# Kernel tuning notes

Measured on AMD Instinct MI355X. Metric: run time of the kernel, lower is better.

## Reference

```python
import jax, jax.numpy as jnp
import numpy as np


def setup_inputs() -> dict:
    key = jax.random.key(0)
    k1, k2, k3 = jax.random.split(key, 3)
    B, N, K = 512, 1024, 64  # batch, seq_len, num_tags
    y_pred = jax.random.normal(k1, (B, N, K), dtype=jnp.float32)
    # glorot-uniform-ish init for the transition matrix
    limit = np.sqrt(6.0 / (K + K)).astype(np.float32)
    trans = jax.random.uniform(k2, (K, K), dtype=jnp.float32, minval=-limit, maxval=limit)
    y_true = jax.random.randint(k3, (B, N), 0, K, dtype=jnp.int32)
    return {"y_pred": y_pred, "trans": trans, "y_true": y_true}


def _crf_loss(y_pred, trans, y_true):
    # mask derived from padding convention: padded frames have logits <= -1e6
    mask = jnp.all(y_pred > -1e6, axis=2, keepdims=True).astype(y_pred.dtype)  # [B,N,1]
    y_pred = y_pred * mask
    m = mask[..., 0]  # [B,N]

    # ---- target (gold-path) score ----
    # point score: emission logits at the gold labels (one-hot einsum == gather)
    point = jnp.sum(
        jnp.take_along_axis(y_pred, y_true[..., None], axis=2)[..., 0] * m, axis=1
    )  # [B]
    # transition score: trans[y_t, y_{t+1}], zeroed where either frame is masked
    tvals = trans[y_true[:, :-1], y_true[:, 1:]] * m[:, :-1] * m[:, 1:]  # [B,N-1]
    target_score = point + jnp.sum(tvals, axis=1)  # [B]

    # ---- log normalizer via forward recursion (logsumexp semiring scan) ----
    init = y_pred[:, 0]  # [B,K]
    emits = jnp.swapaxes(y_pred[:, 1:], 0, 1)  # [N-1,B,K]
    masks = jnp.swapaxes(mask[:, 1:], 0, 1)    # [N-1,B,1]

    def step(alpha, xm):
        emit, mm = xm
        # alpha: [B,K] -> broadcast over next-tag axis with trans [K,K]
        new = jax.nn.logsumexp(alpha[:, :, None] + trans[None], axis=1) + emit
        alpha = mm * new + (1.0 - mm) * alpha
        return alpha, None

    alpha, _ = jax.lax.scan(step, init, (emits, masks))
    log_norm = jax.nn.logsumexp(alpha, axis=1)  # [B]
    return log_norm - target_score


def reference(y_pred, trans, y_true):
    return _crf_loss(y_pred, trans, y_true)
```

## Files before the change

kernel.cpp:

```cpp
#include <hip/hip_runtime.h>
#include <cstdint>
#include <cstddef>


constexpr int Nn = 1024;
constexpr int Kk = 64;
constexpr int P  = 8;

typedef float v2f __attribute__((ext_vector_type(2)));

#define LDS_FENCE() asm volatile("s_waitcnt lgkmcnt(0)" ::: "memory")

__global__ __launch_bounds__(64, 1) void crf_fwd(
    const float* __restrict__ y_pred,
    const float* __restrict__ trans,
    const int*   __restrict__ y_true,
    float* __restrict__ out)
{
    const int b = blockIdx.x;
    const int j = threadIdx.x;

    __shared__ float zbuf[2][Kk];

    const float LOG2E = 1.4426950408889634f;
    const float LN2   = 0.6931471805599453f;

    v2f e2[Kk / 2];
#pragma unroll
    for (int p = 0; p < Kk / 2; ++p) {
        float lo = exp2f(trans[(2 * p)     * Kk + j] * LOG2E);
        float hi = exp2f(trans[(2 * p + 1) * Kk + j] * LOG2E);
        e2[p] = (v2f){lo, hi};
    }

    const float* yp  = y_pred + (size_t)b * Nn * Kk;
    const int*   ytb = y_true + (size_t)b * Nn;

    float emit0 = yp[j];
    bool  m0 = (bool)__all(emit0 > -1000000.0f);
    float a0 = m0 ? emit0 : 0.0f;
    float M0 = __uint_as_float(__builtin_amdgcn_readfirstlane(__float_as_uint(a0)));
    float z  = exp2f((a0 - M0) * LOG2E);

    int   yt0  = ytb[0];
    float pacc = (m0 && j == yt0) ? emit0 : 0.0f;
    float tacc = 0.0f;
    int   S    = 0;
    bool  m_prev = m0;

    float ering[P];
    int   yring[P];
#pragma unroll
    for (int p = 1; p <= P; ++p) {
        ering[p & (P - 1)] = yp[(size_t)p * Kk + j];
        yring[p & (P - 1)] = ytb[p];
    }
    float tvr[2];
    tvr[1] = trans[yt0      * Kk + yring[1]];
    tvr[0] = trans[yring[1] * Kk + yring[2]];

    auto STEP = [&](int t, int slot, int tslot) {
        float emit = ering[slot];
        int   yt   = yring[slot];
        int tt = t + P;
        tt = (tt > Nn - 1) ? (Nn - 1) : tt;
        ering[slot] = yp[(size_t)tt * Kk + j];
        yring[slot] = ytb[tt];

        bool m = (bool)__all(emit > -1000000.0f);

        uint32_t zb0 = __builtin_amdgcn_readfirstlane(__float_as_uint(z));
        int s = (int)((zb0 >> 23) & 0xFF) - 127;

        float pe  = exp2f(emit * LOG2E);
        float tvv = tvr[tslot];
        tvr[tslot] = trans[yring[(slot + 1) & (P - 1)] * Kk +
                           yring[(slot + 2) & (P - 1)]];

        float* zc = zbuf[t & 1];
        zc[j] = z;
        LDS_FENCE();

        v2f acc0 = {0.f, 0.f}, acc1 = {0.f, 0.f};
        v2f acc2 = {0.f, 0.f}, acc3 = {0.f, 0.f};
#pragma unroll
        for (int q = 0; q < 16; q += 2) {
            float4 za = *reinterpret_cast<const float4*>(zc + 4 * q);
            float4 zb = *reinterpret_cast<const float4*>(zc + 4 * q + 4);
            acc0 = __builtin_elementwise_fma((v2f){za.x, za.y}, e2[2 * q],     acc0);
            acc1 = __builtin_elementwise_fma((v2f){za.z, za.w}, e2[2 * q + 1], acc1);
            acc2 = __builtin_elementwise_fma((v2f){zb.x, zb.y}, e2[2 * q + 2], acc2);
            acc3 = __builtin_elementwise_fma((v2f){zb.z, zb.w}, e2[2 * q + 3], acc3);
        }
        v2f accS = (acc0 + acc1) + (acc2 + acc3);
        float dot = accS.x + accS.y;

        float znew = ldexpf(dot * pe, -s);
        z     = m ? znew : z;
        S    += m ? s : 0;
        pacc += (m && j == yt) ? emit : 0.0f;
        tacc += (m && m_prev) ? tvv : 0.0f;
        m_prev = m;
    };

    for (int tb = 0; tb < 127; ++tb) {
        const int tbase = tb * 8;
#pragma unroll
        for (int u = 1; u <= 8; ++u) {
            STEP(tbase + u, u & 7, u & 1);
        }
    }
#pragma unroll
    for (int t = 1017; t < Nn; ++t) {
        STEP(t, t & 7, t & 1);
    }

    float sz = z;
    float sp = pacc;
#pragma unroll
    for (int off = 32; off; off >>= 1) {
        sz += __shfl_xor(sz, off);
        sp += __shfl_xor(sp, off);
    }

    if (j == 0) {
        float log_norm = logf(sz) + (float)S * LN2 + M0;
        out[b] = log_norm - (sp + tacc);
    }
}

extern "C" void kernel_launch(void* const* d_in, const int* in_sizes, int n_in,
                              void* d_out, int out_size, void* d_ws, size_t ws_size,
                              hipStream_t stream) {
    const float* y_pred = (const float*)d_in[0];
    const float* trans  = (const float*)d_in[1];
    const int*   y_true = (const int*)d_in[2];
    float* out = (float*)d_out;

    const int B = 512;
    crf_fwd<<<B, Kk, 0, stream>>>(y_pred, trans, y_true, out);
}
```

Measured before the change: 307.9 us.

## Use fp16 packed dot2 with readlane broadcast instead of LDS matvec

Replaces the per-step LDS store/fence/reload of the alpha vector with a DPP lane-swap that packs neighbouring z values into fp16 pairs, which are broadcast via readlane. The dot against exp(trans) is done with fp16 fdot2. Rescaling by 2^-s is applied before the dot instead of after, so z fits fp16 range. This removes the LDS round-trip latency from the serial recurrence but lowers precision to fp16 for both the transition weights and the state.

```diff
diff --git a/kernel.cpp b/kernel.cpp
--- a/kernel.cpp
+++ b/kernel.cpp
@@ -7,9 +7,27 @@
 constexpr int Kk = 64;
 constexpr int P  = 8;
 
-typedef float v2f __attribute__((ext_vector_type(2)));
+typedef _Float16 v2h __attribute__((ext_vector_type(2)));
 
-#define LDS_FENCE() asm volatile("s_waitcnt lgkmcnt(0)" ::: "memory")
+__device__ __forceinline__ v2h pk_f16(float lo, float hi) {
+    return __builtin_bit_cast(v2h, __builtin_amdgcn_cvt_pkrtz(lo, hi));
+}
+
+__device__ __forceinline__ int lane_xor1(int v) {
+#if __has_builtin(__builtin_amdgcn_mov_dpp)
+    return __builtin_amdgcn_mov_dpp(v, 0xB1, 0xF, 0xF, true);
+#else
+    return __shfl_xor(v, 1);
+#endif
+}
+
+#if __has_builtin(__builtin_amdgcn_fdot2)
+#define DOT2(a, b, c) __builtin_amdgcn_fdot2((a), (b), (c), false)
+#else
+__device__ __forceinline__ float DOT2(v2h a, v2h b, float c) {
+    return c + (float)a.x * (float)b.x + (float)a.y * (float)b.y;
+}
+#endif
 
 __global__ __launch_bounds__(64, 1) void crf_fwd(
     const float* __restrict__ y_pred,
@@ -20,17 +38,15 @@
     const int b = blockIdx.x;
     const int j = threadIdx.x;
 
-    __shared__ float zbuf[2][Kk];
-
     const float LOG2E = 1.4426950408889634f;
     const float LN2   = 0.6931471805599453f;
 
-    v2f e2[Kk / 2];
+    v2h e2h[Kk / 2];
 #pragma unroll
     for (int p = 0; p < Kk / 2; ++p) {
         float lo = exp2f(trans[(2 * p)     * Kk + j] * LOG2E);
         float hi = exp2f(trans[(2 * p + 1) * Kk + j] * LOG2E);
-        e2[p] = (v2f){lo, hi};
+        e2h[p] = pk_f16(lo, hi);
     }
 
     const float* yp  = y_pred + (size_t)b * Nn * Kk;
@@ -77,25 +93,30 @@
         tvr[tslot] = trans[yring[(slot + 1) & (P - 1)] * Kk +
                            yring[(slot + 2) & (P - 1)]];
 
-        float* zc = zbuf[t & 1];
-        zc[j] = z;
-        LDS_FENCE();
+        float zs = ldexpf(z, -s);
+        int   zsb = __builtin_bit_cast(int, zs);
+        int   znb = lane_xor1(zsb);
+        float zn  = __builtin_bit_cast(float, znb);
+        v2h zp = pk_f16(zs, zn);
+        int zi = __builtin_bit_cast(int, zp);
 
-        v2f acc0 = {0.f, 0.f}, acc1 = {0.f, 0.f};
-        v2f acc2 = {0.f, 0.f}, acc3 = {0.f, 0.f};
-#pragma unroll
-        for (int q = 0; q < 16; q += 2) {
-            float4 za = *reinterpret_cast<const float4*>(zc + 4 * q);
-            float4 zb = *reinterpret_cast<const float4*>(zc + 4 * q + 4);
-            acc0 = __builtin_elementwise_fma((v2f){za.x, za.y}, e2[2 * q],     acc0);
-            acc1 = __builtin_elementwise_fma((v2f){za.z, za.w}, e2[2 * q + 1], acc1);
-            acc2 = __builtin_elementwise_fma((v2f){zb.x, zb.y}, e2[2 * q + 2], acc2);
-            acc3 = __builtin_elementwise_fma((v2f){zb.z, zb.w}, e2[2 * q + 3], acc3);
-        }
-        v2f accS = (acc0 + acc1) + (acc2 + acc3);
-        float dot = accS.x + accS.y;
+        float A0 = 0.f, A1 = 0.f, A2 = 0.f, A3 = 0.f;
+        float A4 = 0.f, A5 = 0.f, A6 = 0.f, A7 = 0.f;
+#define DS(k, A) { int sk = __builtin_amdgcn_readlane(zi, 2 * (k));            \
+                   v2h hv = __builtin_bit_cast(v2h, sk);                       \
+                   A = DOT2(hv, e2h[k], A); }
+        DS(0, A0)  DS(1, A1)  DS(2, A2)  DS(3, A3)
+        DS(4, A4)  DS(5, A5)  DS(6, A6)  DS(7, A7)
+        DS(8, A0)  DS(9, A1)  DS(10, A2) DS(11, A3)
+        DS(12, A4) DS(13, A5) DS(14, A6) DS(15, A7)
+        DS(16, A0) DS(17, A1) DS(18, A2) DS(19, A3)
+        DS(20, A4) DS(21, A5) DS(22, A6) DS(23, A7)
+        DS(24, A0) DS(25, A1) DS(26, A2) DS(27, A3)
+        DS(28, A4) DS(29, A5) DS(30, A6) DS(31, A7)
+#undef DS
+        float dot = ((A0 + A1) + (A2 + A3)) + ((A4 + A5) + (A6 + A7));
 
-        float znew = ldexpf(dot * pe, -s);
+        float znew = dot * pe;
         z     = m ? znew : z;
         S    += m ? s : 0;
         pacc += (m && j == yt) ? emit : 0.0f;
```

New measurement: 279.3 us. 1.1x faster.
